# Kernel optimization log

Hardware: AMD Instinct MI355X
Metric: run time of the kernel (lower is better)

Reference implementation:

```python
import jax, jax.numpy as jnp
import numpy as np

OFF_THRESH = 0.5  # specials.OFF_THRESH
INF = 1e10        # specials.INF


def _neighbor_gather(v):
    # v: [B, C, 3, 3, K, Hp, Wp] -> [B, C, 9, K, Hp, Wp]
    # entry (s,t) at output pixel (h,w) reads cell (s,t) of source pixel
    # (h-(s-1), w-(t-1)), i.e. the pixel whose window cell points at (h,w).
    B, C, _, _, K, Hp, Wp = v.shape
    vp = jnp.pad(v, ((0, 0), (0, 0), (0, 0), (0, 0), (0, 0), (1, 1), (1, 1)))
    slabs = [vp[:, :, s, t, :, 2 - s:2 - s + Hp, 2 - t:2 - t + Wp]
             for s in range(3) for t in range(3)]
    return jnp.stack(slabs, axis=2)


def _rays(cam_inv, Hp, Wp):
    # normalized (x/z, y/z) camera rays for padded pixel grid extended by 1
    xs = jnp.arange(-1, Wp + 1, dtype=jnp.float32)
    ys = jnp.arange(-1, Hp + 1, dtype=jnp.float32)
    u, v = jnp.meshgrid(xs, ys)                      # [Hp+2, Wp+2]
    hom = jnp.stack([u, v, jnp.ones_like(u)], 0)     # [3, Hp+2, Wp+2]
    r = jnp.einsum('ij,jhw->ihw', cam_inv, hom)
    return r[:2] / r[2:3]                            # [2, Hp+2, Wp+2]


def _smap_forward(x, cam):
    B = x.shape[0]
    H, W = x.shape[-2], x.shape[-1]
    Hp, Wp = H + 2, W + 2
    # add_pad: zero-pad spatially by 1 (3x3 window)
    xp = jnp.pad(x, ((0, 0), (0, 0), (1, 1), (1, 1)))
    xv, yv, zv, rm = xp[:, None, 0], xp[:, None, 1], xp[:, None, 2], xp[:, None, 3]  # [B,1,Hp,Wp]

    # ---- SMap3x3.forward ----
    cam_inv = jnp.linalg.inv(cam)
    rays = _rays(cam_inv, Hp, Wp)
    zs = jnp.where(zv > 0.0, zv, 1.0)
    px, py = xv / zs, yv / zs                        # projected normalized coords
    costs = []
    for s in range(3):
        for t in range(3):
            rx = rays[0, s:s + Hp, t:t + Wp]
            ry = rays[1, s:s + Hp, t:t + Wp]
            costs.append((px - rx) ** 2 + (py - ry) ** 2)
    key_query = jnp.stack(costs, axis=2)             # [B,1,9,Hp,Wp]

    idx = jnp.argmin(key_query, axis=2)              # argmax(-kq)
    weights_b = jax.nn.one_hot(idx, 9, axis=2, dtype=x.dtype)   # [B,1,9,Hp,Wp]
    valid = (rm > OFF_THRESH) & (zv > 0.0)           # [B,1,Hp,Wp]
    weights_b = jnp.where(valid[:, :, None], weights_b, 0.0)
    temp = jax.nn.one_hot(jnp.full((1,), 4), 9, dtype=x.dtype).reshape(1, 1, 9, 1, 1)
    bad = (rm > OFF_THRESH) & ~(zv > 0.0)
    weights_b = jnp.where(bad[:, :, None], temp, weights_b)

    xyz = jnp.stack([xv, yv, zv], axis=2)            # [B,1,3,Hp,Wp]
    wdet = jax.lax.stop_gradient(weights_b).reshape(B, 1, 3, 3, Hp, Wp)
    new_xyz = jnp.einsum('bcsthw,bczhw->bcstzhw', wdet, xyz)  # [B,1,3,3,3,Hp,Wp]
    weights_b2 = jnp.where(valid[:, :, None], weights_b, temp)
    new_rm = (jax.lax.stop_gradient(weights_b2) * rm[:, :, None]).reshape(B, 1, 3, 3, 1, Hp, Wp)
    nxz = jnp.concatenate([new_xyz, new_rm], axis=4)  # [B,1,3,3,4,Hp,Wp]

    # ---- calculate_weights ----
    zch = jax.lax.stop_gradient(nxz[:, :, :, :, 2:3])           # detached z channel
    gz = _neighbor_gather(zch)                                  # [B,1,9,1,Hp,Wp]
    gz = jnp.where(gz > 0.0, gz, INF)                           # agg(..., factor=INF)
    val = jnp.min(gz, axis=2, keepdims=True)
    sidx = jnp.argmin(gz, axis=2, keepdims=True)
    sidx = jnp.where((val > 0.0) & (val < INF), sidx, 4)
    sel = jax.nn.one_hot(sidx[:, :, 0], 9, axis=2, dtype=x.dtype)  # [B,1,9,1,Hp,Wp]
    gall = _neighbor_gather(nxz)                                # [B,1,9,4,Hp,Wp]
    out = jnp.sum(gall * sel, axis=2)                           # [B,1,4,Hp,Wp]
    # center crop back to original size
    out = out[:, :, :, 1:1 + H, 1:1 + W].reshape(B, 4, H, W)
    return out


def setup_inputs() -> dict:
    key = jax.random.key(0)
    k1, k2, k3 = jax.random.split(key, 3)
    B, H, W = 4, 512, 640
    xy = jax.random.normal(k1, (B, 2, H, W), dtype=jnp.float32)
    z = jax.random.uniform(k2, (B, 1, H, W), minval=0.5, maxval=5.0, dtype=jnp.float32)
    m = jax.random.uniform(k3, (B, 1, H, W), dtype=jnp.float32)
    x = jnp.concatenate([xy, z, m], axis=1)          # channels: x, y, z, mask
    cam = jnp.asarray(np.array([[500.0, 0.0, W / 2.0],
                                [0.0, 500.0, H / 2.0],
                                [0.0, 0.0, 1.0]], dtype=np.float32))
    return {"x": x, "cam": cam}


def reference(x, cam):
    return _smap_forward(x, cam)
```

## Files before the change

kernel.cpp:

```cpp
#include <hip/hip_runtime.h>

#define BT 16
#define HT 18
#define PP 19

__device__ __attribute__((noinline))
int kcode_generic(float px, float py, int gh, int gw,
                  float i00, float i01, float i02,
                  float i10, float i11, float i12,
                  float i20, float i21, float i22, int fastcam)
{
    float A0[3], A1[3], B0[3], B1[3];
    #pragma unroll
    for (int t = 0; t < 3; ++t) {
        const float u = (float)(gw + t);
        A0[t] = __fmul_rn(i00, u);
        A1[t] = __fmul_rn(i10, u);
    }
    #pragma unroll
    for (int s = 0; s < 3; ++s) {
        const float v = (float)(gh + s);
        B0[s] = __fmul_rn(i01, v);
        B1[s] = __fmul_rn(i11, v);
    }
    float best = __builtin_inff();
    int bi = 0;
    #pragma unroll
    for (int n = 0; n < 9; ++n) {
        const int s = n / 3, t = n % 3;
        const float r0 = __fadd_rn(__fadd_rn(A0[t], B0[s]), i02);
        const float r1 = __fadd_rn(__fadd_rn(A1[t], B1[s]), i12);
        float rx, ry;
        if (fastcam) { rx = r0; ry = r1; }
        else {
            const float u = (float)(gw + t), v = (float)(gh + s);
            const float r2 = __fadd_rn(__fadd_rn(__fmul_rn(i20, u), __fmul_rn(i21, v)), i22);
            rx = __fdiv_rn(r0, r2);
            ry = __fdiv_rn(r1, r2);
        }
        const float dx = __fsub_rn(px, rx);
        const float dy = __fsub_rn(py, ry);
        const float c  = __fadd_rn(__fmul_rn(dx, dx), __fmul_rn(dy, dy));
        if (c < best) { best = c; bi = n; }
    }
    return bi;
}

__global__ __launch_bounds__(256, 8) void smap_fused(
    const float* __restrict__ x, const float* __restrict__ cam,
    float* __restrict__ out, int B, int H, int W)
{
    __shared__ float2 szk[HT][PP];

    const int tiles_x = W / BT, tiles_y = H / BT;
    const int ntiles = tiles_x * tiles_y * B;
    int bid = blockIdx.x + tiles_x * (blockIdx.y + tiles_y * blockIdx.z);
    if ((ntiles & 7) == 0) bid = (bid & 7) * (ntiles >> 3) + (bid >> 3);
    const int txt = bid % tiles_x;
    const int rest = bid / tiles_x;
    const int tyt = rest % tiles_y;
    const int b   = rest / tiles_y;

    const int h0 = tyt * BT, w0 = txt * BT;
    const int tx = threadIdx.x;
    const int ty = threadIdx.y;
    const int tid = ty * 16 + tx;

    const float a00 = cam[0], a01 = cam[1], a02 = cam[2];
    const float a10 = cam[3], a11 = cam[4], a12 = cam[5];
    const float a20 = cam[6], a21 = cam[7], a22 = cam[8];
    const float m00 = a11 * a22 - a12 * a21;
    const float m01 = a10 * a22 - a12 * a20;
    const float m02 = a10 * a21 - a11 * a20;
    const float det = a00 * m00 - a01 * m01 + a02 * m02;
    const float i00 = m00 / det;
    const float i01 = (a02 * a21 - a01 * a22) / det;
    const float i02 = (a01 * a12 - a02 * a11) / det;
    const float i10 = (a12 * a20 - a10 * a22) / det;
    const float i11 = (a00 * a22 - a02 * a20) / det;
    const float i12 = (a02 * a10 - a00 * a12) / det;
    const float i20 = m02 / det;
    const float i21 = (a01 * a20 - a00 * a21) / det;
    const float i22 = (a00 * a11 - a01 * a10) / det;

    const bool fastcam = (i20 == 0.0f) && (i21 == 0.0f) && (i22 == 1.0f);
    const bool fastsep = fastcam &&
        (__float_as_uint(i01) == 0u) && (__float_as_uint(i10) == 0u);

    const size_t HW = (size_t)H * W;
    const float* xb = x + (size_t)b * 4 * HW;

    for (int item = tid; item < HT * HT; item += 256) {
        const int i = item / HT, j = item - i * HT;
        const int gh = h0 - 1 + i, gw = w0 - 1 + j;
        float xv = 0.f, yv = 0.f, zv = 0.f, rm = 0.f;
        if (gh >= 0 && gh < H && gw >= 0 && gw < W) {
            const size_t off = (size_t)gh * W + gw;
            xv = xb[off];
            yv = xb[HW + off];
            zv = xb[2 * HW + off];
            rm = xb[3 * HW + off];
        }
        const float zs = (zv > 0.f) ? zv : 1.0f;
        const float px = __fdiv_rn(xv, zs);
        const float py = __fdiv_rn(yv, zs);

        int bi;
        if (fastsep) {
            float f[3], g[3];
            #pragma unroll
            for (int t = 0; t < 3; ++t) {
                const float u  = (float)(gw + t);
                const float rx = __fadd_rn(__fmul_rn(i00, u), i02);
                const float dx = __fsub_rn(px, rx);
                f[t] = __fmul_rn(dx, dx);
            }
            #pragma unroll
            for (int s = 0; s < 3; ++s) {
                const float v  = (float)(gh + s);
                const float ry = __fadd_rn(__fmul_rn(i11, v), i12);
                const float dy = __fsub_rn(py, ry);
                g[s] = __fmul_rn(dy, dy);
            }
            float best = __builtin_inff();
            bi = 0;
            #pragma unroll
            for (int n = 0; n < 9; ++n) {
                const float c = __fadd_rn(f[n % 3], g[n / 3]);
                if (c < best) { best = c; bi = n; }
            }
        } else {
            bi = kcode_generic(px, py, gh, gw, i00, i01, i02,
                               i10, i11, i12, i20, i21, i22, (int)fastcam);
        }

        const bool validp = (rm > 0.5f) && (zv > 0.0f);
        const bool badp   = (rm > 0.5f) && !(zv > 0.0f);
        const int k = validp ? bi : (badp ? 4 : 9);
        szk[i][j] = make_float2(zv, __int_as_float(k));
    }
    __syncthreads();

    float2 cA[3], cB[3], cC[3];
    #pragma unroll
    for (int c = 0; c < 3; ++c) {
        cA[c] = szk[ty][tx + c];
        cB[c] = szk[ty + 1][tx + c];
        cC[c] = szk[ty + 2][tx + c];
    }

    float bz = 1e10f;
    int bli = ty + 1, blj = tx + 1;
    #pragma unroll
    for (int t = 0; t < 3; ++t) {
        const float z = cC[2 - t].x;
        const int   k = __float_as_int(cC[2 - t].y);
        const float cand = (k == t && z > 0.f) ? z : 1e10f;
        if (cand < bz) { bz = cand; bli = ty + 2; blj = tx + 2 - t; }
    }
    #pragma unroll
    for (int t = 0; t < 3; ++t) {
        const float z = cB[2 - t].x;
        const int   k = __float_as_int(cB[2 - t].y);
        const float cand = (k == 3 + t && z > 0.f) ? z : 1e10f;
        if (cand < bz) { bz = cand; bli = ty + 1; blj = tx + 2 - t; }
    }
    #pragma unroll
    for (int t = 0; t < 3; ++t) {
        const float z = cA[2 - t].x;
        const int   k = __float_as_int(cA[2 - t].y);
        const float cand = (k == 6 + t && z > 0.f) ? z : 1e10f;
        if (cand < bz) { bz = cand; bli = ty; blj = tx + 2 - t; }
    }
    const bool found = bz < 1e10f;

    const size_t woff = (size_t)(h0 - 1 + bli) * W + (w0 - 1 + blj);
    const float vx  = xb[woff];
    const float vy  = xb[HW + woff];
    const float vrm = xb[3 * HW + woff];

    float ox, oy, oz, orm;
    if (found) {
        ox = vx; oy = vy; oz = bz; orm = vrm;
    } else {
        const int   kc = __float_as_int(cB[1].y);
        const float zc = cB[1].x;
        const bool  k4 = (kc == 4);
        const bool  validp = (vrm > 0.5f) && (zc > 0.f);
        ox = k4 ? vx : 0.f;
        oy = k4 ? vy : 0.f;
        oz = k4 ? zc : 0.f;
        orm = (k4 || !validp) ? vrm : 0.f;
    }

    const int h = h0 + ty, w = w0 + tx;
    const size_t obase = (size_t)b * 4 * HW + (size_t)h * W + w;
    __builtin_nontemporal_store(ox,  &out[obase]);
    __builtin_nontemporal_store(oy,  &out[obase + HW]);
    __builtin_nontemporal_store(oz,  &out[obase + 2 * HW]);
    __builtin_nontemporal_store(orm, &out[obase + 3 * HW]);
}

extern "C" void kernel_launch(void* const* d_in, const int* in_sizes, int n_in,
                              void* d_out, int out_size, void* d_ws, size_t ws_size,
                              hipStream_t stream) {
    const float* x   = (const float*)d_in[0];
    const float* cam = (const float*)d_in[1];
    float* out = (float*)d_out;
    const int H = 512, W = 640;
    const int B = in_sizes[0] / (4 * H * W);
    dim3 block(16, 16);
    dim3 grid(W / BT, H / BT, B);
    hipLaunchKernelGGL(smap_fused, grid, block, 0, stream, x, cam, out, B, H, W);
}
```

Measured before the change: 20.44 us.

## Enlarge tile to 32x32 with 4 rows per thread and rolling register window

The spatial tile grows from 16x16 to 32x32, so the halo shrinks relative to the tile and less per-pixel code computation is repeated at tile borders. The block becomes 32x8 and each thread now produces 4 output rows, carrying the 3x3 window down in registers so each step needs only one new shared-memory row. The cost is a larger shared-memory footprint per block and a quarter as many blocks, which may lower occupancy and latency hiding for the dependent gathers from global memory.

```diff
diff --git a/kernel.cpp b/kernel.cpp
--- a/kernel.cpp
+++ b/kernel.cpp
@@ -1,8 +1,8 @@
 #include <hip/hip_runtime.h>
 
-#define BT 16
-#define HT 18
-#define PP 19
+#define BT 32
+#define HT (BT + 2)
+#define PP (HT + 1)
 
 __device__ __attribute__((noinline))
 int kcode_generic(float px, float py, int gh, int gw,
@@ -64,7 +64,7 @@
     const int h0 = tyt * BT, w0 = txt * BT;
     const int tx = threadIdx.x;
     const int ty = threadIdx.y;
-    const int tid = ty * 16 + tx;
+    const int tid = ty * 32 + tx;
 
     const float a00 = cam[0], a01 = cam[1], a02 = cam[2];
     const float a10 = cam[3], a11 = cam[4], a12 = cam[5];
@@ -141,64 +141,74 @@
     }
     __syncthreads();
 
-    float2 cA[3], cB[3], cC[3];
+    const int rbase = 4 * ty;
+    float2 rA[3], rB[3], rC[3];
     #pragma unroll
     for (int c = 0; c < 3; ++c) {
-        cA[c] = szk[ty][tx + c];
-        cB[c] = szk[ty + 1][tx + c];
-        cC[c] = szk[ty + 2][tx + c];
-    }
-
-    float bz = 1e10f;
-    int bli = ty + 1, blj = tx + 1;
-    #pragma unroll
-    for (int t = 0; t < 3; ++t) {
-        const float z = cC[2 - t].x;
-        const int   k = __float_as_int(cC[2 - t].y);
-        const float cand = (k == t && z > 0.f) ? z : 1e10f;
-        if (cand < bz) { bz = cand; bli = ty + 2; blj = tx + 2 - t; }
-    }
-    #pragma unroll
-    for (int t = 0; t < 3; ++t) {
-        const float z = cB[2 - t].x;
-        const int   k = __float_as_int(cB[2 - t].y);
-        const float cand = (k == 3 + t && z > 0.f) ? z : 1e10f;
-        if (cand < bz) { bz = cand; bli = ty + 1; blj = tx + 2 - t; }
-    }
-    #pragma unroll
-    for (int t = 0; t < 3; ++t) {
-        const float z = cA[2 - t].x;
-        const int   k = __float_as_int(cA[2 - t].y);
-        const float cand = (k == 6 + t && z > 0.f) ? z : 1e10f;
-        if (cand < bz) { bz = cand; bli = ty; blj = tx + 2 - t; }
-    }
-    const bool found = bz < 1e10f;
-
-    const size_t woff = (size_t)(h0 - 1 + bli) * W + (w0 - 1 + blj);
-    const float vx  = xb[woff];
-    const float vy  = xb[HW + woff];
-    const float vrm = xb[3 * HW + woff];
-
-    float ox, oy, oz, orm;
-    if (found) {
-        ox = vx; oy = vy; oz = bz; orm = vrm;
-    } else {
-        const int   kc = __float_as_int(cB[1].y);
-        const float zc = cB[1].x;
-        const bool  k4 = (kc == 4);
-        const bool  validp = (vrm > 0.5f) && (zc > 0.f);
-        ox = k4 ? vx : 0.f;
-        oy = k4 ? vy : 0.f;
-        oz = k4 ? zc : 0.f;
-        orm = (k4 || !validp) ? vrm : 0.f;
-    }
-
-    const int h = h0 + ty, w = w0 + tx;
-    const size_t obase = (size_t)b * 4 * HW + (size_t)h * W + w;
-    __builtin_nontemporal_store(ox,  &out[obase]);
-    __builtin_nontemporal_store(oy,  &out[obase + HW]);
-    __builtin_nontemporal_store(oz,  &out[obase + 2 * HW]);
-    __builtin_nontemporal_store(orm, &out[obase + 3 * HW]);
+        rA[c] = szk[rbase][tx + c];
+        rB[c] = szk[rbase + 1][tx + c];
+    }
+
+    #pragma unroll
+    for (int q = 0; q < 4; ++q) {
+        const int rq = rbase + q;
+        #pragma unroll
+        for (int c = 0; c < 3; ++c) rC[c] = szk[rq + 2][tx + c];
+
+        float bz = 1e10f;
+        int bli = rq + 1, blj = tx + 1;
+        #pragma unroll
+        for (int t = 0; t < 3; ++t) {
+            const float z = rC[2 - t].x;
+            const int   k = __float_as_int(rC[2 - t].y);
+            const float cand = (k == t && z > 0.f) ? z : 1e10f;
+            if (cand < bz) { bz = cand; bli = rq + 2; blj = tx + 2 - t; }
+        }
+        #pragma unroll
+        for (int t = 0; t < 3; ++t) {
+            const float z = rB[2 - t].x;
+            const int   k = __float_as_int(rB[2 - t].y);
+            const float cand = (k == 3 + t && z > 0.f) ? z : 1e10f;
+            if (cand < bz) { bz = cand; bli = rq + 1; blj = tx + 2 - t; }
+        }
+        #pragma unroll
+        for (int t = 0; t < 3; ++t) {
+            const float z = rA[2 - t].x;
+            const int   k = __float_as_int(rA[2 - t].y);
+            const float cand = (k == 6 + t && z > 0.f) ? z : 1e10f;
+            if (cand < bz) { bz = cand; bli = rq; blj = tx + 2 - t; }
+        }
+        const bool found = bz < 1e10f;
+
+        const size_t woff = (size_t)(h0 - 1 + bli) * W + (w0 - 1 + blj);
+        const float vx  = xb[woff];
+        const float vy  = xb[HW + woff];
+        const float vrm = xb[3 * HW + woff];
+
+        float ox, oy, oz, orm;
+        if (found) {
+            ox = vx; oy = vy; oz = bz; orm = vrm;
+        } else {
+            const int   kc = __float_as_int(rB[1].y);
+            const float zc = rB[1].x;
+            const bool  k4 = (kc == 4);
+            const bool  validp = (vrm > 0.5f) && (zc > 0.f);
+            ox = k4 ? vx : 0.f;
+            oy = k4 ? vy : 0.f;
+            oz = k4 ? zc : 0.f;
+            orm = (k4 || !validp) ? vrm : 0.f;
+        }
+
+        const int h = h0 + rq, w = w0 + tx;
+        const size_t obase = (size_t)b * 4 * HW + (size_t)h * W + w;
+        __builtin_nontemporal_store(ox,  &out[obase]);
+        __builtin_nontemporal_store(oy,  &out[obase + HW]);
+        __builtin_nontemporal_store(oz,  &out[obase + 2 * HW]);
+        __builtin_nontemporal_store(orm, &out[obase + 3 * HW]);
+
+        #pragma unroll
+        for (int c = 0; c < 3; ++c) { rA[c] = rB[c]; rB[c] = rC[c]; }
+    }
 }
 
 extern "C" void kernel_launch(void* const* d_in, const int* in_sizes, int n_in,
@@ -209,7 +219,7 @@
     float* out = (float*)d_out;
     const int H = 512, W = 640;
     const int B = in_sizes[0] / (4 * H * W);
-    dim3 block(16, 16);
+    dim3 block(32, 8);
     dim3 grid(W / BT, H / BT, B);
     hipLaunchKernelGGL(smap_fused, grid, block, 0, stream, x, cam, out, B, H, W);
 }
```

Result: faster. 16.43 us, median of 2 (-19.6%).
